# Performance work log

Hardware: AMD Instinct MI355X
Metric: run time of the kernel (lower is better)

The kernel has to match this reference:

```python
import jax, jax.numpy as jnp
import numpy as np

B = 512
IN_FEATURES = 512
OUT_FEATURES = 100
KERNEL_DIM = 5


def setup_inputs() -> dict:
    key = jax.random.key(0)
    kx, kT = jax.random.split(key)
    x = jax.random.normal(kx, (B, IN_FEATURES), dtype=jnp.float32)
    # nn.init.normal_(T, 0, 1)
    T = jax.random.normal(kT, (IN_FEATURES, OUT_FEATURES, KERNEL_DIM), dtype=jnp.float32)
    return {"x": x, "T": T}


def reference(x, T):
    # matrices = x @ T.view(in, out*k) -> (B, out, k)
    M = jnp.einsum('bi,iok->bok', x, T)  # [B, O, K]
    # pairwise L1 distance over kernel dim: norm[i, j, o] = sum_k |M[i,o,k] - M[j,o,k]|
    norm = jnp.abs(M[:, None, :, :] - M[None, :, :, :]).sum(-1)  # [B, B, O]
    expnorm = jnp.exp(-norm)
    # sum over first batch axis; subtract 1 to remove self-term (exp(0) = 1)
    o_b = expnorm.sum(0) - 1.0  # [B, O]
    return o_b
```

## Files before the change

### kernel.cpp

```cpp
#include <hip/hip_runtime.h>
#include <math.h>


#define NB    512
#define NIN   512
#define NOUT  100
#define KDIM  5
#define NCOL  (NOUT*KDIM)
#define KZ    8
#define MP_ELEMS (NB*NCOL)
#define M8_LD 800

__global__ __launch_bounds__(256) void gemm_kernel(const float* __restrict__ A,
                                                   const float* __restrict__ Bm,
                                                   float* __restrict__ Mpart) {
    __shared__ float As[64][68];
    __shared__ float Bs[64][68];

    const int tx = threadIdx.x;
    const int ty = threadIdx.y;
    const int tid = ty * 16 + tx;
    const int bn = blockIdx.x * 64;
    const int bm = blockIdx.y * 64;
    const int kz = blockIdx.z;
    const int kt = kz * 64;

    #pragma unroll
    for (int l = 0; l < 4; ++l) {
        int idx = tid + l * 256;
        int row = idx >> 4, q = idx & 15;
        float4 v = *reinterpret_cast<const float4*>(&A[(bm + row) * NIN + kt + q * 4]);
        *reinterpret_cast<float4*>(&As[row][q * 4]) = v;
    }
    #pragma unroll
    for (int l = 0; l < 4; ++l) {
        int idx = tid + l * 256;
        int row = idx >> 4, q = idx & 15;
        int col = bn + q * 4;
        float4 v;
        if (col + 3 < NCOL) {
            v = *reinterpret_cast<const float4*>(&Bm[(kt + row) * NCOL + col]);
        } else {
            v.x = (col + 0 < NCOL) ? Bm[(kt + row) * NCOL + col + 0] : 0.f;
            v.y = (col + 1 < NCOL) ? Bm[(kt + row) * NCOL + col + 1] : 0.f;
            v.z = (col + 2 < NCOL) ? Bm[(kt + row) * NCOL + col + 2] : 0.f;
            v.w = (col + 3 < NCOL) ? Bm[(kt + row) * NCOL + col + 3] : 0.f;
        }
        *reinterpret_cast<float4*>(&Bs[row][q * 4]) = v;
    }
    __syncthreads();

    float acc[4][4];
    #pragma unroll
    for (int i = 0; i < 4; ++i)
        #pragma unroll
        for (int j = 0; j < 4; ++j) acc[i][j] = 0.f;

    #pragma unroll 4
    for (int k = 0; k < 64; ++k) {
        float a[4], b[4];
        #pragma unroll
        for (int i = 0; i < 4; ++i) a[i] = As[ty * 4 + i][k];
        #pragma unroll
        for (int j = 0; j < 4; ++j) b[j] = Bs[k][tx * 4 + j];
        #pragma unroll
        for (int i = 0; i < 4; ++i)
            #pragma unroll
            for (int j = 0; j < 4; ++j) acc[i][j] += a[i] * b[j];
    }

    float* C = Mpart + kz * MP_ELEMS;
    #pragma unroll
    for (int i = 0; i < 4; ++i) {
        int row = bm + ty * 4 + i;
        int col0 = bn + tx * 4;
        if (col0 + 3 < NCOL) {
            float4 v = make_float4(acc[i][0], acc[i][1], acc[i][2], acc[i][3]);
            *reinterpret_cast<float4*>(&C[row * NCOL + col0]) = v;
        } else {
            #pragma unroll
            for (int j = 0; j < 4; ++j)
                if (col0 + j < NCOL) C[row * NCOL + col0 + j] = acc[i][j];
        }
    }
}

__global__ __launch_bounds__(256) void reduce_kernel(const float* __restrict__ Mpart,
                                                     float* __restrict__ M8) {
    const unsigned gtid = blockIdx.x * 256 + threadIdx.x;
    for (unsigned n = gtid; n < MP_ELEMS; n += 64000) {
        unsigned b = n / NCOL;
        unsigned c = n - b * NCOL;
        unsigned o = c / KDIM;
        unsigned k = c - o * KDIM;
        float s = 0.f;
        #pragma unroll
        for (int z = 0; z < KZ; ++z) s += Mpart[z * MP_ELEMS + n];
        M8[b * M8_LD + o * 8 + k] = s;
    }
}

__global__ __launch_bounds__(256) void pairwise_kernel(const float* __restrict__ M8,
                                                       float* __restrict__ out) {
    __shared__ float Ms[NB * 8];
    __shared__ float partial[256];

    const int o   = blockIdx.x;
    const int jc  = blockIdx.y;
    const int tid = threadIdx.x;

    for (int b = tid; b < NB; b += 256) {
        const float* src = M8 + b * M8_LD + o * 8;
        float4 v0 = *reinterpret_cast<const float4*>(src);
        float4 v1 = *reinterpret_cast<const float4*>(src + 4);
        *reinterpret_cast<float4*>(&Ms[b * 8])     = v0;
        *reinterpret_cast<float4*>(&Ms[b * 8 + 4]) = v1;
    }
    __syncthreads();

    const int j  = jc * 64 + (tid & 63);
    const int i0 = (tid >> 6) * 128;

    const float4 jv = *reinterpret_cast<const float4*>(&Ms[j * 8]);
    const float  j4 = Ms[j * 8 + 4];

    float acc = 0.0f;
    #pragma unroll 4
    for (int i = i0; i < i0 + 128; ++i) {
        float4 v = *reinterpret_cast<const float4*>(&Ms[i * 8]);
        float v4 = Ms[i * 8 + 4];
        float norm = fabsf(v.x - jv.x) + fabsf(v.y - jv.y) + fabsf(v.z - jv.z)
                   + fabsf(v.w - jv.w) + fabsf(v4 - j4);
        acc += __expf(-norm);
    }

    partial[tid] = acc;
    __syncthreads();

    if (tid < 64) {
        float tot = partial[tid] + partial[tid + 64] + partial[tid + 128]
                  + partial[tid + 192] - 1.0f;
        out[(jc * 64 + tid) * NOUT + o] = tot;
    }
}

extern "C" void kernel_launch(void* const* d_in, const int* in_sizes, int n_in,
                              void* d_out, int out_size, void* d_ws, size_t ws_size,
                              hipStream_t stream) {
    const float* x = (const float*)d_in[0];
    const float* T = (const float*)d_in[1];
    float* Mpart = (float*)d_ws;
    float* M8    = (float*)d_ws + KZ * MP_ELEMS;
    float* out   = (float*)d_out;

    gemm_kernel<<<dim3(8, 8, KZ), dim3(16, 16), 0, stream>>>(x, T, Mpart);
    reduce_kernel<<<250, 256, 0, stream>>>(Mpart, M8);
    pairwise_kernel<<<dim3(NOUT, 8), 256, 0, stream>>>(M8, out);
}
```

Before: 85.52 us.

## Fuse split-K reduction into GEMM via atomics and widen pairwise grid

Removes the separate reduce kernel and the split-K partial buffer: each GEMM block atomically adds its partial tile directly into the padded M8 layout, which is zeroed with a memset first. The GEMM inner loop now reads shared memory with float4 loads over four k-steps at once. The pairwise kernel moves from 64 to 32 j-values per block, doubling the grid to 16 column chunks per output, and uses a more coalesced half-row staging load. Atomics add contention and make the summation order nondeterministic, and the memset is an extra launch.

```diff
diff --git a/kernel.cpp b/kernel.cpp
--- a/kernel.cpp
+++ b/kernel.cpp
@@ -8,12 +8,11 @@
 #define KDIM  5
 #define NCOL  (NOUT*KDIM)
 #define KZ    8
-#define MP_ELEMS (NB*NCOL)
 #define M8_LD 800
 
 __global__ __launch_bounds__(256) void gemm_kernel(const float* __restrict__ A,
                                                    const float* __restrict__ Bm,
-                                                   float* __restrict__ Mpart) {
+                                                   float* __restrict__ M8) {
     __shared__ float As[64][68];
     __shared__ float Bs[64][68];
 
@@ -22,8 +21,7 @@
     const int tid = ty * 16 + tx;
     const int bn = blockIdx.x * 64;
     const int bm = blockIdx.y * 64;
-    const int kz = blockIdx.z;
-    const int kt = kz * 64;
+    const int kt = blockIdx.z * 64;
 
     #pragma unroll
     for (int l = 0; l < 4; ++l) {
@@ -57,46 +55,38 @@
         for (int j = 0; j < 4; ++j) acc[i][j] = 0.f;
 
     #pragma unroll 4
-    for (int k = 0; k < 64; ++k) {
-        float a[4], b[4];
-        #pragma unroll
-        for (int i = 0; i < 4; ++i) a[i] = As[ty * 4 + i][k];
-        #pragma unroll
-        for (int j = 0; j < 4; ++j) b[j] = Bs[k][tx * 4 + j];
+    for (int k = 0; k < 64; k += 4) {
+        float4 a4[4], b4[4];
         #pragma unroll
         for (int i = 0; i < 4; ++i)
+            a4[i] = *reinterpret_cast<const float4*>(&As[ty * 4 + i][k]);
+        #pragma unroll
+        for (int kk = 0; kk < 4; ++kk)
+            b4[kk] = *reinterpret_cast<const float4*>(&Bs[k + kk][tx * 4]);
+        #pragma unroll
+        for (int kk = 0; kk < 4; ++kk) {
+            const float* bp = reinterpret_cast<const float*>(&b4[kk]);
             #pragma unroll
-            for (int j = 0; j < 4; ++j) acc[i][j] += a[i] * b[j];
+            for (int i = 0; i < 4; ++i) {
+                const float a = reinterpret_cast<const float*>(&a4[i])[kk];
+                #pragma unroll
+                for (int j = 0; j < 4; ++j) acc[i][j] += a * bp[j];
+            }
+        }
     }
 
-    float* C = Mpart + kz * MP_ELEMS;
     #pragma unroll
     for (int i = 0; i < 4; ++i) {
-        int row = bm + ty * 4 + i;
-        int col0 = bn + tx * 4;
-        if (col0 + 3 < NCOL) {
-            float4 v = make_float4(acc[i][0], acc[i][1], acc[i][2], acc[i][3]);
-            *reinterpret_cast<float4*>(&C[row * NCOL + col0]) = v;
-        } else {
-            #pragma unroll
-            for (int j = 0; j < 4; ++j)
-                if (col0 + j < NCOL) C[row * NCOL + col0 + j] = acc[i][j];
+        const int row = bm + ty * 4 + i;
+        #pragma unroll
+        for (int j = 0; j < 4; ++j) {
+            const int col = bn + tx * 4 + j;
+            if (col < NCOL) {
+                const int o  = col / KDIM;
+                const int kk = col - o * KDIM;
+                unsafeAtomicAdd(&M8[row * M8_LD + o * 8 + kk], acc[i][j]);
+            }
         }
-    }
-}
-
-__global__ __launch_bounds__(256) void reduce_kernel(const float* __restrict__ Mpart,
-                                                     float* __restrict__ M8) {
-    const unsigned gtid = blockIdx.x * 256 + threadIdx.x;
-    for (unsigned n = gtid; n < MP_ELEMS; n += 64000) {
-        unsigned b = n / NCOL;
-        unsigned c = n - b * NCOL;
-        unsigned o = c / KDIM;
-        unsigned k = c - o * KDIM;
-        float s = 0.f;
-        #pragma unroll
-        for (int z = 0; z < KZ; ++z) s += Mpart[z * MP_ELEMS + n];
-        M8[b * M8_LD + o * 8 + k] = s;
     }
 }
 
@@ -109,24 +99,25 @@
     const int jc  = blockIdx.y;
     const int tid = threadIdx.x;
 
-    for (int b = tid; b < NB; b += 256) {
-        const float* src = M8 + b * M8_LD + o * 8;
-        float4 v0 = *reinterpret_cast<const float4*>(src);
-        float4 v1 = *reinterpret_cast<const float4*>(src + 4);
-        *reinterpret_cast<float4*>(&Ms[b * 8])     = v0;
-        *reinterpret_cast<float4*>(&Ms[b * 8 + 4]) = v1;
+    {
+        const int half = tid & 1;
+        for (int b = tid >> 1; b < NB; b += 128) {
+            const float* src = M8 + b * M8_LD + o * 8 + half * 4;
+            *reinterpret_cast<float4*>(&Ms[b * 8 + half * 4]) =
+                *reinterpret_cast<const float4*>(src);
+        }
     }
     __syncthreads();
 
-    const int j  = jc * 64 + (tid & 63);
-    const int i0 = (tid >> 6) * 128;
+    const int j  = jc * 32 + (tid & 31);
+    const int i0 = (tid >> 5) * 64;
 
     const float4 jv = *reinterpret_cast<const float4*>(&Ms[j * 8]);
     const float  j4 = Ms[j * 8 + 4];
 
     float acc = 0.0f;
-    #pragma unroll 4
-    for (int i = i0; i < i0 + 128; ++i) {
+    #pragma unroll 8
+    for (int i = i0; i < i0 + 64; ++i) {
         float4 v = *reinterpret_cast<const float4*>(&Ms[i * 8]);
         float v4 = Ms[i * 8 + 4];
         float norm = fabsf(v.x - jv.x) + fabsf(v.y - jv.y) + fabsf(v.z - jv.z)
@@ -137,10 +128,11 @@
     partial[tid] = acc;
     __syncthreads();
 
-    if (tid < 64) {
-        float tot = partial[tid] + partial[tid + 64] + partial[tid + 128]
-                  + partial[tid + 192] - 1.0f;
-        out[(jc * 64 + tid) * NOUT + o] = tot;
+    if (tid < 32) {
+        float tot = -1.0f;
+        #pragma unroll
+        for (int s = 0; s < 8; ++s) tot += partial[tid + s * 32];
+        out[(jc * 32 + tid) * NOUT + o] = tot;
     }
 }
 
@@ -149,11 +141,10 @@
                               hipStream_t stream) {
     const float* x = (const float*)d_in[0];
     const float* T = (const float*)d_in[1];
-    float* Mpart = (float*)d_ws;
-    float* M8    = (float*)d_ws + KZ * MP_ELEMS;
-    float* out   = (float*)d_out;
+    float* M8  = (float*)d_ws;
+    float* out = (float*)d_out;
 
-    gemm_kernel<<<dim3(8, 8, KZ), dim3(16, 16), 0, stream>>>(x, T, Mpart);
-    reduce_kernel<<<250, 256, 0, stream>>>(Mpart, M8);
-    pairwise_kernel<<<dim3(NOUT, 8), 256, 0, stream>>>(M8, out);
+    hipMemsetAsync(M8, 0, NB * M8_LD * sizeof(float), stream);
+    gemm_kernel<<<dim3(8, 8, KZ), dim3(16, 16), 0, stream>>>(x, T, M8);
+    pairwise_kernel<<<dim3(NOUT, 16), 256, 0, stream>>>(M8, out);
 }
```

After: 122.7 us. +43.5%, slower.
